# Kernel tuning notes

Measured on AMD Instinct MI355X. Metric: run time of the kernel, lower is better.

Reference implementation:

```python
import jax, jax.numpy as jnp
import numpy as np

H_IMG = 64; W_IMG = 64; N = H_IMG * W_IMG
IN_CH = 128; HID = 8; HEADS = 4; OUT_CH = 64; BATCH = 16
NEG_SLOPE = 0.2


def _build_graph():
    # Faithful replication of GATHead._construct_graph (n_neighbor=3 -> 5x5 unfold windows)
    m = np.arange(N).reshape(H_IMG, W_IMG)
    pad = np.full((H_IMG + 6, W_IMG + 6), -1, dtype=np.int64)
    pad[3:3 + H_IMG, 3:3 + W_IMG] = m
    win = np.lib.stride_tricks.sliding_window_view(pad, (5, 5))  # (h+2, w+2, 5, 5)
    lookup = win.reshape(-1, 25)[:N]                             # first N rows used
    adj = np.zeros((N, N), dtype=bool)
    rows = np.repeat(np.arange(N), 25)
    cols = lookup.reshape(-1)
    valid = cols >= 0
    adj[rows[valid], cols[valid]] = True
    adj = adj | adj.T                       # dgl.to_bidirected (simple graph)
    u, v = np.nonzero(adj)
    src = np.concatenate([u, np.arange(N)]).astype(np.int32)  # dgl.add_self_loop appends (i,i)
    dst = np.concatenate([v, np.arange(N)]).astype(np.int32)
    return src, dst


def setup_inputs() -> dict:
    key = jax.random.key(0)
    ks = jax.random.split(key, 9)
    src, dst = _build_graph()
    s = 0.1
    return {
        "x": jax.random.normal(ks[0], (BATCH, IN_CH, H_IMG, W_IMG), jnp.float32),
        "W1": jax.random.normal(ks[1], (IN_CH, HEADS * HID), jnp.float32) * s,
        "al1": jax.random.normal(ks[2], (1, HEADS, HID), jnp.float32) * s,
        "ar1": jax.random.normal(ks[3], (1, HEADS, HID), jnp.float32) * s,
        "b1": jax.random.normal(ks[4], (HEADS * HID,), jnp.float32) * s,
        "W2": jax.random.normal(ks[5], (HEADS * HID, OUT_CH), jnp.float32) * s,
        "al2": jax.random.normal(ks[6], (1, 1, OUT_CH), jnp.float32) * s,
        "ar2": jax.random.normal(ks[7], (1, 1, OUT_CH), jnp.float32) * s,
        "b2": jax.random.normal(ks[8], (OUT_CH,), jnp.float32) * s,
        "src": jnp.asarray(src),
        "dst": jnp.asarray(dst),
    }


def _gat_conv(x, W, al, ar, b, src, dst, heads, dout):
    # DGL GATConv: linear proj, per-edge LeakyReLU attention logits, per-dst edge softmax, scatter-sum
    feat = (x @ W).reshape(-1, heads, dout)          # (N, H, D)
    el = jnp.sum(feat * al, axis=-1)                 # (N, H)
    er = jnp.sum(feat * ar, axis=-1)                 # (N, H)
    e = jax.nn.leaky_relu(el[src] + er[dst], NEG_SLOPE)  # (E, H)
    emax = jax.ops.segment_max(e, dst, num_segments=N)
    ex = jnp.exp(e - emax[dst])
    denom = jax.ops.segment_sum(ex, dst, num_segments=N)
    a = ex / denom[dst]                              # (E, H) edge-softmax coeffs
    out = jax.ops.segment_sum(a[:, :, None] * feat[src], dst, num_segments=N)  # (N, H, D)
    return out + b.reshape(1, heads, dout)


def _mish(x):
    return x * jnp.tanh(jax.nn.softplus(x))


def reference(x, W1, al1, ar1, b1, W2, al2, ar2, b2, src, dst):
    xb = x.reshape(BATCH, IN_CH, N).transpose(0, 2, 1)  # b c h w -> b (h w) c

    def single(xi):
        h = _gat_conv(xi, W1, al1, ar1, b1, src, dst, HEADS, HID)   # (N, 4, 8)
        h = _mish(h).reshape(N, HEADS * HID)                        # merge 'n c heads -> n (c heads)'
        return _gat_conv(h, W2, al2, ar2, b2, src, dst, 1, OUT_CH)  # (N, 1, OUT_CH)

    out = jax.vmap(single)(xb)                                      # (B, N, 1, OUT_CH)
    # readout: b (h w) d1 d2 -> b (d1 d2) h w
    return out.reshape(BATCH, H_IMG, W_IMG, OUT_CH).transpose(0, 3, 1, 2)
```

## Files before the change

kernel.cpp:

```cpp
#include <hip/hip_runtime.h>
#include <hip/hip_bf16.h>

#define N_NODES 4096
#define BATCH 16
#define IN_CH 128
#define HID 8
#define HEADS 4
#define F1 (HEADS*HID)
#define OUT_CH 64
#define MAXD 64

__device__ __forceinline__ int node_swz(int bid) {
    return (bid & 7) * 512 + (bid >> 3);
}

__global__ void k_init(int* cursor) {
    int i = blockIdx.x * 256 + threadIdx.x;
    if (i < N_NODES) cursor[i] = 0;
}

__global__ void k_fill(const int* __restrict__ srcA, const int* __restrict__ dstA, int E,
                       int* cursor, int* nbrp) {
    int e = blockIdx.x * 256 + threadIdx.x;
    if (e < E) {
        int n = dstA[e];
        int pos = atomicAdd(&cursor[n], 1);
        nbrp[(n << 6) + pos] = srcA[e];
    }
}

__global__ __launch_bounds__(256) void k_feat1(const float* __restrict__ x,
                                               const float* __restrict__ W1,
                                               const float* __restrict__ al1,
                                               const float* __restrict__ ar1,
                                               float* __restrict__ feat1,
                                               float* __restrict__ el1,
                                               float* __restrict__ er1) {
    __shared__ float lW1[IN_CH * F1];
    __shared__ float lal[F1], lar[F1];
    __shared__ float lt[64 * 33];
    __shared__ float lel[64 * 4], ler[64 * 4];
    int t = threadIdx.x;
    for (int i = t; i < IN_CH * F1; i += 256) lW1[i] = W1[i];
    if (t < F1) { lal[t] = al1[t]; lar[t] = ar1[t]; }
    __syncthreads();

    int b = blockIdx.y;
    int n0 = blockIdx.x * 64;
    int q = t >> 6;
    int nl = t & 63;
    int n = n0 + nl;
    const float* xp = x + (size_t)b * (IN_CH * N_NODES) + n;
    const float* wq = lW1 + q * HID;

    float acc[HID];
    #pragma unroll
    for (int i = 0; i < HID; i++) acc[i] = 0.f;
    #pragma unroll 4
    for (int c = 0; c < IN_CH; c++) {
        float xv = xp[(size_t)c * N_NODES];
        #pragma unroll
        for (int i = 0; i < HID; i++) acc[i] += xv * wq[c * F1 + i];
    }

    float el = 0.f, er = 0.f;
    #pragma unroll
    for (int i = 0; i < HID; i++) {
        el += acc[i] * lal[q * HID + i];
        er += acc[i] * lar[q * HID + i];
    }
    lel[nl * 4 + q] = el;
    ler[nl * 4 + q] = er;

    #pragma unroll
    for (int i = 0; i < HID; i++) lt[nl * 33 + q * HID + i] = acc[i];
    __syncthreads();

    float* fp = feat1 + (size_t)n0 * (BATCH * F1) + b * F1;
    #pragma unroll
    for (int k = 0; k < 8; k++) {
        int idx = k * 256 + t;
        int nn = idx >> 5, f = idx & 31;
        fp[nn * (BATCH * F1) + f] = lt[nn * 33 + f];
    }
    if (t < 64) {
        ((float4*)el1)[(n0 + t) * BATCH + b] = *(float4*)&lel[t * 4];
        ((float4*)er1)[(n0 + t) * BATCH + b] = *(float4*)&ler[t * 4];
    }
}

__global__ __launch_bounds__(256) void k_gat1f(const float* __restrict__ feat1,
                                               const float* __restrict__ el1,
                                               const float* __restrict__ er1,
                                               const int* __restrict__ nbrp,
                                               const int* __restrict__ deg,
                                               const float* __restrict__ b1v,
                                               const float* __restrict__ W2,
                                               const float* __restrict__ al2,
                                               const float* __restrict__ ar2,
                                               float* __restrict__ feat2,
                                               float* __restrict__ el2,
                                               float* __restrict__ er2) {
    __shared__ float lw[MAXD * 64];
    __shared__ float lae[2 * OUT_CH];
    __shared__ float lh[BATCH * F1];
    __shared__ float lb1[F1];
    int t = threadIdx.x;
    int n = node_swz(blockIdx.x);
    if (t < 2 * OUT_CH) lae[t] = (t < OUT_CH) ? al2[t] : ar2[t - OUT_CH];
    if (t < F1) lb1[t] = b1v[t];

    int dg = deg[n];
    int dgc8 = (dg + 7) & ~7;
    const int* nb = nbrp + (n << 6);

    float ern = er1[(n << 6) + (t & 63)];
    for (int r = 0; r * 4 < dgc8; r++) {
        int idx = r * 256 + t;
        int j = idx >> 6;
        int s = (j < dg) ? nb[j] : n;
        float e = el1[(s << 6) + (idx & 63)] + ern;
        e = (e > 0.f) ? e : 0.2f * e;
        lw[idx] = (j < dg) ? __expf(e) : 0.f;
    }
    __syncthreads();

    int b = t >> 4, c2 = t & 15;
    int woff = (b << 2) + (c2 >> 2);
    int t2 = t << 1;
    float ax = 0.f, ay = 0.f, wsum = 0.f;
    for (int g = 0; g < MAXD / 8; g++) {
        if (g * 8 >= dg) break;
        #pragma unroll
        for (int u = 0; u < 8; u++) {
            int j = g * 8 + u;
            int s = (j < dg) ? nb[j] : n;
            float w = lw[(j << 6) + woff];
            wsum += w;
            float2 f = *(const float2*)&feat1[(s << 9) + t2];
            ax += w * f.x; ay += w * f.y;
        }
    }
    float inv = 1.f / wsum;
    float v0 = ax * inv + lb1[c2 * 2];
    float v1 = ay * inv + lb1[c2 * 2 + 1];
    float e0 = __expf(v0), e1 = __expf(v1);
    float p0 = e0 * (e0 + 2.f), p1 = e1 * (e1 + 2.f);
    lh[b * F1 + c2 * 2]     = v0 * p0 / (p0 + 2.f);
    lh[b * F1 + c2 * 2 + 1] = v1 * p1 / (p1 + 2.f);
    __syncthreads();

    int c4 = t & 15;
    float hreg[F1];
    #pragma unroll
    for (int k = 0; k < F1; k++) hreg[k] = lh[b * F1 + k];
    float4 acc = {0.f, 0.f, 0.f, 0.f};
    #pragma unroll
    for (int k = 0; k < F1; k++) {
        float4 w4 = *(const float4*)&W2[k * OUT_CH + c4 * 4];
        acc.x += hreg[k] * w4.x; acc.y += hreg[k] * w4.y;
        acc.z += hreg[k] * w4.z; acc.w += hreg[k] * w4.w;
    }
    *(float4*)&feat2[(n << 10) + (t << 2)] = acc;

    float4 a4 = *(float4*)&lae[c4 * 4];
    float4 r4 = *(float4*)&lae[OUT_CH + c4 * 4];
    float pl = acc.x * a4.x + acc.y * a4.y + acc.z * a4.z + acc.w * a4.w;
    float pr = acc.x * r4.x + acc.y * r4.y + acc.z * r4.z + acc.w * r4.w;
    #pragma unroll
    for (int off = 1; off < 16; off <<= 1) {
        pl += __shfl_xor(pl, off, 64);
        pr += __shfl_xor(pr, off, 64);
    }
    if (c4 == 0) { el2[(n << 4) + b] = pl; er2[(n << 4) + b] = pr; }
}

__global__ __launch_bounds__(256) void k_gat2(const float* __restrict__ feat2,
                                              const float* __restrict__ el2,
                                              const float* __restrict__ er2,
                                              const int* __restrict__ nbrp,
                                              const int* __restrict__ deg,
                                              const float* __restrict__ b2v,
                                              float* __restrict__ out2) {
    __shared__ float lw2[MAXD * BATCH];
    int t = threadIdx.x;
    int n = node_swz(blockIdx.x);
    int dg = deg[n];
    int dgc8 = (dg + 7) & ~7;
    const int* nb = nbrp + (n << 6);

    float ern = er2[(n << 4) + (t & 15)];
    for (int r = 0; r * 16 < dgc8; r++) {
        int idx = r * 256 + t;
        int j = idx >> 4;
        int s = (j < dg) ? nb[j] : n;
        float e = el2[(s << 4) + (idx & 15)] + ern;
        e = (e > 0.f) ? e : 0.2f * e;
        lw2[idx] = (j < dg) ? __expf(e) : 0.f;
    }
    __syncthreads();

    int b = t >> 4, c4 = t & 15;
    int t4 = t << 2;
    float4 acc = {0.f, 0.f, 0.f, 0.f};
    float den = 0.f;
    for (int g = 0; g < MAXD / 8; g++) {
        if (g * 8 >= dg) break;
        #pragma unroll
        for (int u = 0; u < 8; u++) {
            int j = g * 8 + u;
            int s = (j < dg) ? nb[j] : n;
            float w = lw2[(j << 4) + b];
            den += w;
            float4 f = *(const float4*)&feat2[(s << 10) + t4];
            acc.x += w * f.x; acc.y += w * f.y; acc.z += w * f.z; acc.w += w * f.w;
        }
    }
    float inv = 1.f / den;
    float4 bb = *(const float4*)&b2v[c4 * 4];
    float4 o = { acc.x * inv + bb.x, acc.y * inv + bb.y,
                 acc.z * inv + bb.z, acc.w * inv + bb.w };
    *(float4*)&out2[(n << 10) + t4] = o;
}

__global__ __launch_bounds__(256) void k_trans(const float* __restrict__ out2,
                                               float* __restrict__ out) {
    __shared__ float tile[64][65];
    int t = threadIdx.x;
    int b = blockIdx.y;
    int n0 = blockIdx.x * 64;
    int i = t >> 2;
    int c0 = (t & 3) * 4;
    #pragma unroll
    for (int p = 0; p < 4; p++) {
        int c = c0 + p * 16;
        float4 v = *(const float4*)&out2[(size_t)(n0 + i) * (BATCH * OUT_CH) + b * OUT_CH + c];
        tile[i][c] = v.x; tile[i][c + 1] = v.y; tile[i][c + 2] = v.z; tile[i][c + 3] = v.w;
    }
    __syncthreads();
    int nl = t & 63;
    int cw = t >> 6;
    #pragma unroll
    for (int q = 0; q < 16; q++) {
        int c = q * 4 + cw;
        out[(size_t)(b * OUT_CH + c) * N_NODES + n0 + nl] = tile[nl][c];
    }
}

extern "C" void kernel_launch(void* const* d_in, const int* in_sizes, int n_in,
                              void* d_out, int out_size, void* d_ws, size_t ws_size,
                              hipStream_t stream) {
    const float* x   = (const float*)d_in[0];
    const float* W1  = (const float*)d_in[1];
    const float* al1 = (const float*)d_in[2];
    const float* ar1 = (const float*)d_in[3];
    const float* b1v = (const float*)d_in[4];
    const float* W2  = (const float*)d_in[5];
    const float* al2 = (const float*)d_in[6];
    const float* ar2 = (const float*)d_in[7];
    const float* b2v = (const float*)d_in[8];
    const int* srcA  = (const int*)d_in[9];
    const int* dstA  = (const int*)d_in[10];
    int E = in_sizes[9];

    char* ws = (char*)d_ws;
    int*   cursor = (int*)(ws);
    int*   nbrp   = (int*)(ws + 16384);
    float* feat1  = (float*)(ws + 1064960);
    float* el1    = (float*)(ws + 9453568);
    float* er1    = (float*)(ws + 10502144);
    float* feat2  = (float*)(ws + 19939328);
    float* el2    = (float*)(ws + 36716544);
    float* er2    = (float*)(ws + 36978688);
    float* out2   = feat1;

    float* out = (float*)d_out;
    dim3 blk(256);

    k_init<<<dim3(16), blk, 0, stream>>>(cursor);
    k_fill<<<dim3((E + 255) / 256), blk, 0, stream>>>(srcA, dstA, E, cursor, nbrp);

    k_feat1<<<dim3(N_NODES / 64, BATCH), blk, 0, stream>>>(x, W1, al1, ar1, feat1, el1, er1);
    k_gat1f<<<dim3(N_NODES), blk, 0, stream>>>(feat1, el1, er1, nbrp, cursor, b1v,
                                               W2, al2, ar2, feat2, el2, er2);

    k_gat2 <<<dim3(N_NODES), blk, 0, stream>>>(feat2, el2, er2, nbrp, cursor, b2v, out2);

    k_trans<<<dim3(N_NODES / 64, BATCH), blk, 0, stream>>>(out2, out);
}
```

Before: 211.0 us.

## Defer W2 projection past layer-2 aggregation and fold attention vectors into W2

The layer-2 linear projection is moved after the neighbour aggregation, which is valid because aggregation is linear. Layer 2 now gathers 32-wide hidden features instead of 64-wide projected features, roughly halving gather traffic, and the intermediate buffer shrinks. The attention logits are computed with small precomputed W2·al2 and W2·ar2 vectors from a new tiny kernel. The edge loops are also fully unrolled in fixed chunks of 16 guarded by degree checks, which adds code size and register pressure.

Result: slower. 224.8 us (+6.5%).

```diff
diff --git a/kernel.cpp b/kernel.cpp
--- a/kernel.cpp
+++ b/kernel.cpp
@@ -27,6 +27,17 @@
         int pos = atomicAdd(&cursor[n], 1);
         nbrp[(n << 6) + pos] = srcA[e];
     }
+}
+
+__global__ void k_prep(const float* __restrict__ W2, const float* __restrict__ al2,
+                       const float* __restrict__ ar2, float* __restrict__ wlr) {
+    int t = threadIdx.x;
+    int k = t & 31;
+    const float* a = (t < 32) ? al2 : ar2;
+    float s = 0.f;
+    #pragma unroll 8
+    for (int c = 0; c < OUT_CH; c++) s += W2[k * OUT_CH + c] * a[c];
+    wlr[((t < 32) ? 0 : 32) + k] = s;
 }
 
 __global__ __launch_bounds__(256) void k_feat1(const float* __restrict__ x,
@@ -95,33 +106,36 @@
                                                const int* __restrict__ nbrp,
                                                const int* __restrict__ deg,
                                                const float* __restrict__ b1v,
-                                               const float* __restrict__ W2,
-                                               const float* __restrict__ al2,
-                                               const float* __restrict__ ar2,
-                                               float* __restrict__ feat2,
+                                               const float* __restrict__ wlr,
+                                               float* __restrict__ h1,
                                                float* __restrict__ el2,
                                                float* __restrict__ er2) {
     __shared__ float lw[MAXD * 64];
-    __shared__ float lae[2 * OUT_CH];
-    __shared__ float lh[BATCH * F1];
-    __shared__ float lb1[F1];
     int t = threadIdx.x;
     int n = node_swz(blockIdx.x);
-    if (t < 2 * OUT_CH) lae[t] = (t < OUT_CH) ? al2[t] : ar2[t - OUT_CH];
-    if (t < F1) lb1[t] = b1v[t];
-
     int dg = deg[n];
-    int dgc8 = (dg + 7) & ~7;
     const int* nb = nbrp + (n << 6);
 
     float ern = er1[(n << 6) + (t & 63)];
-    for (int r = 0; r * 4 < dgc8; r++) {
+    #pragma unroll
+    for (int r = 0; r < 8; r++) {
         int idx = r * 256 + t;
         int j = idx >> 6;
         int s = (j < dg) ? nb[j] : n;
-        float e = el1[(s << 6) + (idx & 63)] + ern;
+        float e = el1[(s << 6) + (t & 63)] + ern;
         e = (e > 0.f) ? e : 0.2f * e;
         lw[idx] = (j < dg) ? __expf(e) : 0.f;
+    }
+    if (dg > 32) {
+        #pragma unroll
+        for (int r = 8; r < 16; r++) {
+            int idx = r * 256 + t;
+            int j = idx >> 6;
+            int s = (j < dg) ? nb[j] : n;
+            float e = el1[(s << 6) + (t & 63)] + ern;
+            e = (e > 0.f) ? e : 0.2f * e;
+            lw[idx] = (j < dg) ? __expf(e) : 0.f;
+        }
     }
     __syncthreads();
 
@@ -129,98 +143,129 @@
     int woff = (b << 2) + (c2 >> 2);
     int t2 = t << 1;
     float ax = 0.f, ay = 0.f, wsum = 0.f;
-    for (int g = 0; g < MAXD / 8; g++) {
-        if (g * 8 >= dg) break;
-        #pragma unroll
-        for (int u = 0; u < 8; u++) {
-            int j = g * 8 + u;
-            int s = (j < dg) ? nb[j] : n;
-            float w = lw[(j << 6) + woff];
-            wsum += w;
-            float2 f = *(const float2*)&feat1[(s << 9) + t2];
-            ax += w * f.x; ay += w * f.y;
-        }
-    }
+#define G1_EDGE(j) { \
+        int s = ((j) < dg) ? nb[j] : n; \
+        float w = lw[((j) << 6) + woff]; \
+        wsum += w; \
+        float2 f = *(const float2*)&feat1[(s << 9) + t2]; \
+        ax += w * f.x; ay += w * f.y; }
+    #pragma unroll
+    for (int j = 0; j < 16; j++) G1_EDGE(j)
+    if (dg > 16) {
+        #pragma unroll
+        for (int j = 16; j < 32; j++) G1_EDGE(j)
+    }
+    if (dg > 32) {
+        #pragma unroll
+        for (int j = 32; j < 48; j++) G1_EDGE(j)
+    }
+    if (dg > 48) {
+        #pragma unroll
+        for (int j = 48; j < 64; j++) G1_EDGE(j)
+    }
+#undef G1_EDGE
+
     float inv = 1.f / wsum;
-    float v0 = ax * inv + lb1[c2 * 2];
-    float v1 = ay * inv + lb1[c2 * 2 + 1];
+    float2 bb = *(const float2*)&b1v[c2 * 2];
+    float v0 = ax * inv + bb.x;
+    float v1 = ay * inv + bb.y;
     float e0 = __expf(v0), e1 = __expf(v1);
     float p0 = e0 * (e0 + 2.f), p1 = e1 * (e1 + 2.f);
-    lh[b * F1 + c2 * 2]     = v0 * p0 / (p0 + 2.f);
-    lh[b * F1 + c2 * 2 + 1] = v1 * p1 / (p1 + 2.f);
-    __syncthreads();
-
-    int c4 = t & 15;
-    float hreg[F1];
-    #pragma unroll
-    for (int k = 0; k < F1; k++) hreg[k] = lh[b * F1 + k];
-    float4 acc = {0.f, 0.f, 0.f, 0.f};
-    #pragma unroll
-    for (int k = 0; k < F1; k++) {
-        float4 w4 = *(const float4*)&W2[k * OUT_CH + c4 * 4];
-        acc.x += hreg[k] * w4.x; acc.y += hreg[k] * w4.y;
-        acc.z += hreg[k] * w4.z; acc.w += hreg[k] * w4.w;
-    }
-    *(float4*)&feat2[(n << 10) + (t << 2)] = acc;
-
-    float4 a4 = *(float4*)&lae[c4 * 4];
-    float4 r4 = *(float4*)&lae[OUT_CH + c4 * 4];
-    float pl = acc.x * a4.x + acc.y * a4.y + acc.z * a4.z + acc.w * a4.w;
-    float pr = acc.x * r4.x + acc.y * r4.y + acc.z * r4.z + acc.w * r4.w;
+    float o0 = v0 * p0 / (p0 + 2.f);
+    float o1 = v1 * p1 / (p1 + 2.f);
+    *(float2*)&h1[(n << 9) + t2] = make_float2(o0, o1);
+
+    float2 l2 = *(const float2*)&wlr[c2 * 2];
+    float2 r2 = *(const float2*)&wlr[32 + c2 * 2];
+    float pl = o0 * l2.x + o1 * l2.y;
+    float pr = o0 * r2.x + o1 * r2.y;
     #pragma unroll
     for (int off = 1; off < 16; off <<= 1) {
         pl += __shfl_xor(pl, off, 64);
         pr += __shfl_xor(pr, off, 64);
     }
-    if (c4 == 0) { el2[(n << 4) + b] = pl; er2[(n << 4) + b] = pr; }
-}
-
-__global__ __launch_bounds__(256) void k_gat2(const float* __restrict__ feat2,
+    if (c2 == 0) { el2[(n << 4) + b] = pl; er2[(n << 4) + b] = pr; }
+}
+
+__global__ __launch_bounds__(256) void k_gat2(const float* __restrict__ h1,
                                               const float* __restrict__ el2,
                                               const float* __restrict__ er2,
                                               const int* __restrict__ nbrp,
                                               const int* __restrict__ deg,
+                                              const float* __restrict__ W2,
                                               const float* __restrict__ b2v,
                                               float* __restrict__ out2) {
     __shared__ float lw2[MAXD * BATCH];
+    __shared__ float lagg[BATCH * 33];
     int t = threadIdx.x;
     int n = node_swz(blockIdx.x);
     int dg = deg[n];
-    int dgc8 = (dg + 7) & ~7;
     const int* nb = nbrp + (n << 6);
 
     float ern = er2[(n << 4) + (t & 15)];
-    for (int r = 0; r * 16 < dgc8; r++) {
+    #pragma unroll
+    for (int r = 0; r < 2; r++) {
         int idx = r * 256 + t;
         int j = idx >> 4;
         int s = (j < dg) ? nb[j] : n;
-        float e = el2[(s << 4) + (idx & 15)] + ern;
+        float e = el2[(s << 4) + (t & 15)] + ern;
         e = (e > 0.f) ? e : 0.2f * e;
         lw2[idx] = (j < dg) ? __expf(e) : 0.f;
     }
-    __syncthreads();
-
-    int b = t >> 4, c4 = t & 15;
-    int t4 = t << 2;
-    float4 acc = {0.f, 0.f, 0.f, 0.f};
-    float den = 0.f;
-    for (int g = 0; g < MAXD / 8; g++) {
-        if (g * 8 >= dg) break;
-        #pragma unroll
-        for (int u = 0; u < 8; u++) {
-            int j = g * 8 + u;
+    if (dg > 32) {
+        #pragma unroll
+        for (int r = 2; r < 4; r++) {
+            int idx = r * 256 + t;
+            int j = idx >> 4;
             int s = (j < dg) ? nb[j] : n;
-            float w = lw2[(j << 4) + b];
-            den += w;
-            float4 f = *(const float4*)&feat2[(s << 10) + t4];
-            acc.x += w * f.x; acc.y += w * f.y; acc.z += w * f.z; acc.w += w * f.w;
+            float e = el2[(s << 4) + (t & 15)] + ern;
+            e = (e > 0.f) ? e : 0.2f * e;
+            lw2[idx] = (j < dg) ? __expf(e) : 0.f;
         }
     }
+    __syncthreads();
+
+    int b = t >> 4, c2 = t & 15;
+    int t2 = t << 1;
+    float ax = 0.f, ay = 0.f, den = 0.f;
+#define G2_EDGE(j) { \
+        int s = ((j) < dg) ? nb[j] : n; \
+        float w = lw2[((j) << 4) + b]; \
+        den += w; \
+        float2 f = *(const float2*)&h1[(s << 9) + t2]; \
+        ax += w * f.x; ay += w * f.y; }
+    #pragma unroll
+    for (int j = 0; j < 16; j++) G2_EDGE(j)
+    if (dg > 16) {
+        #pragma unroll
+        for (int j = 16; j < 32; j++) G2_EDGE(j)
+    }
+    if (dg > 32) {
+        #pragma unroll
+        for (int j = 32; j < 48; j++) G2_EDGE(j)
+    }
+    if (dg > 48) {
+        #pragma unroll
+        for (int j = 48; j < 64; j++) G2_EDGE(j)
+    }
+#undef G2_EDGE
+
     float inv = 1.f / den;
-    float4 bb = *(const float4*)&b2v[c4 * 4];
-    float4 o = { acc.x * inv + bb.x, acc.y * inv + bb.y,
-                 acc.z * inv + bb.z, acc.w * inv + bb.w };
-    *(float4*)&out2[(n << 10) + t4] = o;
+    lagg[b * 33 + c2 * 2]     = ax * inv;
+    lagg[b * 33 + c2 * 2 + 1] = ay * inv;
+    __syncthreads();
+
+    float4 bb = *(const float4*)&b2v[c2 * 4];
+    float4 acc = bb;
+    const float* ag = &lagg[b * 33];
+    #pragma unroll
+    for (int k = 0; k < F1; k++) {
+        float hk = ag[k];
+        float4 w4 = *(const float4*)&W2[k * OUT_CH + c2 * 4];
+        acc.x += hk * w4.x; acc.y += hk * w4.y;
+        acc.z += hk * w4.z; acc.w += hk * w4.w;
+    }
+    *(float4*)&out2[(n << 10) + (t << 2)] = acc;
 }
 
 __global__ __launch_bounds__(256) void k_trans(const float* __restrict__ out2,
@@ -269,9 +314,10 @@
     float* feat1  = (float*)(ws + 1064960);
     float* el1    = (float*)(ws + 9453568);
     float* er1    = (float*)(ws + 10502144);
-    float* feat2  = (float*)(ws + 19939328);
+    float* h1     = (float*)(ws + 19939328);
     float* el2    = (float*)(ws + 36716544);
     float* er2    = (float*)(ws + 36978688);
+    float* wlr    = (float*)(ws + 37240832);
     float* out2   = feat1;
 
     float* out = (float*)d_out;
@@ -279,12 +325,13 @@
 
     k_init<<<dim3(16), blk, 0, stream>>>(cursor);
     k_fill<<<dim3((E + 255) / 256), blk, 0, stream>>>(srcA, dstA, E, cursor, nbrp);
+    k_prep<<<dim3(1), dim3(64), 0, stream>>>(W2, al2, ar2, wlr);
 
     k_feat1<<<dim3(N_NODES / 64, BATCH), blk, 0, stream>>>(x, W1, al1, ar1, feat1, el1, er1);
-    k_gat1f<<<dim3(N_NODES), blk, 0, stream>>>(feat1, el1, er1, nbrp, cursor, b1v,
-                                               W2, al2, ar2, feat2, el2, er2);
-
-    k_gat2 <<<dim3(N_NODES), blk, 0, stream>>>(feat2, el2, er2, nbrp, cursor, b2v, out2);
+    k_gat1f<<<dim3(N_NODES), blk, 0, stream>>>(feat1, el1, er1, nbrp, cursor, b1v, wlr,
+                                               h1, el2, er2);
+
+    k_gat2 <<<dim3(N_NODES), blk, 0, stream>>>(h1, el2, er2, nbrp, cursor, W2, b2v, out2);
 
     k_trans<<<dim3(N_NODES / 64, BATCH), blk, 0, stream>>>(out2, out);
 }
```
